# Performance work log

Measured on AMD Instinct MI355X. Metric: run time of the kernel, lower is better.

## Reference

```python
import jax, jax.numpy as jnp
import numpy as np

B, Q, C, V = 512, 100, 81, 117  # batch, queries, obj classes (80+no-object), verbs
THRES, ALPHA, BETA = 0.7, 1.0, 0.5


def setup_inputs() -> dict:
    key = jax.random.key(0)
    k1, k2, k3, k4, k5, k6 = jax.random.split(key, 6)
    out_obj_logits = jax.random.normal(k1, (B, Q, C), jnp.float32)
    out_verb_logits = jax.random.normal(k2, (B, Q, V), jnp.float32)
    out_sub_boxes = jax.random.uniform(k3, (B, Q, 4), jnp.float32)
    out_obj_boxes = jax.random.uniform(k4, (B, Q, 4), jnp.float32)
    # correct_mat: binary verb-object compatibility [V, C-1] + ones column for no-object slot -> [V, C]
    cm = (jax.random.uniform(k5, (V, C - 1)) < 0.3).astype(jnp.float32)
    correct_mat = jnp.concatenate([cm, jnp.ones((V, 1), jnp.float32)], axis=1)
    target_sizes = jax.random.randint(k6, (B, 2), 480, 1334).astype(jnp.int64)
    return {
        'out_obj_logits': out_obj_logits,
        'out_verb_logits': out_verb_logits,
        'out_sub_boxes': out_sub_boxes,
        'out_obj_boxes': out_obj_boxes,
        'correct_mat': correct_mat,
        'target_sizes': target_sizes,
    }


def _box_cxcywh_to_xyxy(b):
    cx, cy, w, h = b[..., 0], b[..., 1], b[..., 2], b[..., 3]
    return jnp.stack([cx - 0.5 * w, cy - 0.5 * h, cx + 0.5 * w, cy + 0.5 * h], axis=-1)


def _pairwise_iou(boxes):  # boxes [Q,4] xyxy (pixel coords, +1 convention as in source)
    x1, y1, x2, y2 = boxes[:, 0], boxes[:, 1], boxes[:, 2], boxes[:, 3]
    area = (x2 - x1 + 1.0) * (y2 - y1 + 1.0)
    xx1 = jnp.maximum(x1[:, None], x1[None, :])
    yy1 = jnp.maximum(y1[:, None], y1[None, :])
    xx2 = jnp.minimum(x2[:, None], x2[None, :])
    yy2 = jnp.minimum(y2[:, None], y2[None, :])
    w = jnp.maximum(0.0, xx2 - xx1 + 1.0)
    h = jnp.maximum(0.0, yy2 - yy1 + 1.0)
    inter = w * h
    union = area[:, None] + area[None, :] - inter
    return inter / union


def _nms_one_image(sub_b, obj_b, obj_lab, max_scores):
    # Greedy pairwise triplet NMS. Grouping key in the source degenerates to the
    # object label alone (subject cat is constant, verb-label string identical),
    # so suppression applies only between detections with the same object label.
    order = jnp.argsort(-max_scores)
    sb, ob, lab = sub_b[order], obj_b[order], obj_lab[order]
    ovr = jnp.power(_pairwise_iou(sb), ALPHA) * jnp.power(_pairwise_iou(ob), BETA)
    upper = jnp.triu(jnp.ones((Q, Q), bool), 1)
    sup_mat = upper & (lab[:, None] == lab[None, :]) & (ovr > THRES)

    def body(i, supp):
        return supp | (sup_mat[i] & jnp.logical_not(supp[i]))

    supp = jax.lax.fori_loop(0, Q, body, jnp.zeros((Q,), bool))
    keep = jnp.zeros((Q,), bool).at[order].set(jnp.logical_not(supp))
    return keep  # in original query order


def reference(out_obj_logits, out_verb_logits, out_sub_boxes, out_obj_boxes, correct_mat, target_sizes):
    obj_prob = jax.nn.softmax(out_obj_logits, axis=-1)
    obj_scores = obj_prob[..., :-1].max(axis=-1)            # [B,Q]
    obj_labels = obj_prob[..., :-1].argmax(axis=-1)         # [B,Q]
    verb_scores = jax.nn.sigmoid(out_verb_logits)           # [B,Q,V]

    ts = target_sizes.astype(jnp.float32)
    img_h, img_w = ts[:, 0], ts[:, 1]
    scale_fct = jnp.stack([img_w, img_h, img_w, img_h], axis=1)  # [B,4]
    sub_boxes = _box_cxcywh_to_xyxy(out_sub_boxes) * scale_fct[:, None, :]
    obj_boxes = _box_cxcywh_to_xyxy(out_obj_boxes) * scale_fct[:, None, :]

    # masks[b,q,v] = correct_mat[v, obj_labels[b,q]]
    masks = correct_mat.T[obj_labels]                        # [B,Q,V]
    hoi_scores = verb_scores * obj_scores[..., None] * masks

    max_scores = hoi_scores.max(axis=-1)                     # [B,Q]
    keep = jax.vmap(_nms_one_image)(sub_boxes, obj_boxes, obj_labels, max_scores)
    return hoi_scores, obj_labels, sub_boxes, obj_boxes, keep
```

## Files before the change

kernel.cpp:

```cpp
#include <hip/hip_runtime.h>
#include <math.h>

#define Bn 512
#define Qn 100
#define Cn 81
#define Vn 117
#define NQ (Bn * Qn)

#define OFF_HOI  0
#define OFF_LAB  (NQ * Vn)
#define OFF_SUB  (OFF_LAB + NQ)
#define OFF_OBJ  (OFF_SUB + NQ * 4)
#define OFF_KEEP (OFF_OBJ + NQ * 4)

__device__ __forceinline__ float frcp(float x) { return __builtin_amdgcn_rcpf(x); }

__global__ __launch_bounds__(512) void hoi_fused(
    const float* __restrict__ obj_logits,
    const float* __restrict__ verb_logits,
    const float* __restrict__ sub_boxes,
    const float* __restrict__ obj_boxes,
    const float* __restrict__ cm,
    const int*   __restrict__ target_sizes,
    float* __restrict__ out)
{
    __shared__ __align__(16) char smem[37920];
    __shared__ float sc[Qn];
    __shared__ int   labs[Qn];

    float*      CM    = (float*)smem;
    float4*     Ssub  = (float4*)smem;
    float4*     Sobj  = Ssub + Qn;
    float4*     Smeta = Sobj + Qn;
    ulonglong2* RR    = (ulonglong2*)(Smeta + Qn);

    const int tid = threadIdx.x;
    const int b   = blockIdx.x;

    {
        const float4* c4 = (const float4*)cm;
        float4* C4 = (float4*)CM;
        for (int i = tid; i < (Vn * Cn) / 4; i += 512) C4[i] = c4[i];
        if (tid == 0) CM[Vn * Cn - 1] = cm[Vn * Cn - 1];
    }

    float4 rs = make_float4(0.f, 0.f, 0.f, 0.f), ro = rs;
    if (tid < Qn) {
        const float ih = (float)target_sizes[2 * b + 0];
        const float iw = (float)target_sizes[2 * b + 1];
        const int idx = b * Qn + tid;
        float4 bx = ((const float4*)sub_boxes)[idx];
        rs.x = (bx.x - 0.5f * bx.z) * iw;
        rs.y = (bx.y - 0.5f * bx.w) * ih;
        rs.z = (bx.x + 0.5f * bx.z) * iw;
        rs.w = (bx.y + 0.5f * bx.w) * ih;
        ((float4*)(out + OFF_SUB))[idx] = rs;
        bx = ((const float4*)obj_boxes)[idx];
        ro.x = (bx.x - 0.5f * bx.z) * iw;
        ro.y = (bx.y - 0.5f * bx.w) * ih;
        ro.z = (bx.x + 0.5f * bx.z) * iw;
        ro.w = (bx.y + 0.5f * bx.w) * ih;
        ((float4*)(out + OFF_OBJ))[idx] = ro;
    }
    __syncthreads();

    {
        const int t = tid & 15;
        const int g = tid >> 4;
        for (int q = g; q < Qn; q += 32) {
            const size_t idx = (size_t)b * Qn + q;
            const float* lg = obj_logits + idx * Cn;
            const float* vl = verb_logits + idx * Vn;

            float l0 = lg[t], l1 = lg[t + 16], l2 = lg[t + 32],
                  l3 = lg[t + 48], l4 = lg[t + 64], l5 = lg[80];
            float w0 = vl[t], w1 = vl[t + 16], w2 = vl[t + 32], w3 = vl[t + 48],
                  w4 = vl[t + 64], w5 = vl[t + 80], w6 = vl[t + 96];
            float w7 = (t < 5) ? vl[112 + t] : 0.f;

            float v = l0; int vid = t;
            if (l1 > v) { v = l1; vid = t + 16; }
            if (l2 > v) { v = l2; vid = t + 32; }
            if (l3 > v) { v = l3; vid = t + 48; }
            if (l4 > v) { v = l4; vid = t + 64; }
            #pragma unroll
            for (int o = 8; o; o >>= 1) {
                float ov = __shfl_xor(v, o, 64);
                int   oi = __shfl_xor(vid, o, 64);
                if (ov > v || (ov == v && oi < vid)) { v = ov; vid = oi; }
            }

            float e = __expf(l0) + __expf(l1) + __expf(l2) + __expf(l3) + __expf(l4);
            #pragma unroll
            for (int o = 8; o; o >>= 1) e += __shfl_xor(e, o, 64);
            e += __expf(l5);

            const int   label     = vid;
            const float obj_score = __expf(v) * frcp(e);

            float* hout = out + OFF_HOI + idx * Vn;
            const float* cmrow = CM + label;
            float mx = 0.f;
            {
                float h;
                h = frcp(1.f + __expf(-w0)) * obj_score * cmrow[(t      ) * Cn];
                hout[t      ] = h; mx = fmaxf(mx, h);
                h = frcp(1.f + __expf(-w1)) * obj_score * cmrow[(t +  16) * Cn];
                hout[t +  16] = h; mx = fmaxf(mx, h);
                h = frcp(1.f + __expf(-w2)) * obj_score * cmrow[(t +  32) * Cn];
                hout[t +  32] = h; mx = fmaxf(mx, h);
                h = frcp(1.f + __expf(-w3)) * obj_score * cmrow[(t +  48) * Cn];
                hout[t +  48] = h; mx = fmaxf(mx, h);
                h = frcp(1.f + __expf(-w4)) * obj_score * cmrow[(t +  64) * Cn];
                hout[t +  64] = h; mx = fmaxf(mx, h);
                h = frcp(1.f + __expf(-w5)) * obj_score * cmrow[(t +  80) * Cn];
                hout[t +  80] = h; mx = fmaxf(mx, h);
                h = frcp(1.f + __expf(-w6)) * obj_score * cmrow[(t +  96) * Cn];
                hout[t +  96] = h; mx = fmaxf(mx, h);
                if (t < 5) {
                    h = frcp(1.f + __expf(-w7)) * obj_score * cmrow[(112 + t) * Cn];
                    hout[112 + t] = h; mx = fmaxf(mx, h);
                }
            }
            #pragma unroll
            for (int o = 8; o; o >>= 1) mx = fmaxf(mx, __shfl_xor(mx, o, 64));

            if (t == 0) {
                out[OFF_LAB + idx] = (float)label;
                sc[q]   = mx;
                labs[q] = label;
            }
        }
    }
    __syncthreads();

    if (tid < Qn) {
        const float kv = sc[tid];
        int r = 0;
        #pragma unroll 4
        for (int j = 0; j < Qn; j++) {
            float sj = sc[j];
            r += (sj > kv) || (sj == kv && j < tid);
        }
        Ssub[r] = rs;
        Sobj[r] = ro;
        Smeta[r] = make_float4((rs.z - rs.x + 1.f) * (rs.w - rs.y + 1.f),
                               (ro.z - ro.x + 1.f) * (ro.w - ro.y + 1.f),
                               (float)labs[tid], (float)tid);
    }
    __syncthreads();

    {
        const int tc   = tid & 127;
        const int uq   = tid >> 7;
        const int lane = tid & 63;
        const int sub  = (tid >> 6) & 1;
        const bool jv  = (tc < Qn);

        float4 js = make_float4(0.f, 0.f, 0.f, 0.f), jo = js, jm = js;
        if (jv) { js = Ssub[tc]; jo = Sobj[tc]; jm = Smeta[tc]; }

        const int i0 = 25 * uq;
        const int i1 = (25 * uq + 25 < Qn - 1) ? 25 * uq + 25 : Qn - 1;
        for (int i = i0; i < i1; i++) {
            float4 is = Ssub[i], io = Sobj[i], im = Smeta[i];
            float ww = fmaxf(0.f, fminf(is.z, js.z) - fmaxf(is.x, js.x) + 1.f);
            float hh = fmaxf(0.f, fminf(is.w, js.w) - fmaxf(is.y, js.y) + 1.f);
            float inter = ww * hh;
            float iou_s = inter / (im.x + jm.x - inter);
            ww = fmaxf(0.f, fminf(io.z, jo.z) - fmaxf(io.x, jo.x) + 1.f);
            hh = fmaxf(0.f, fminf(io.w, jo.w) - fmaxf(io.y, jo.y) + 1.f);
            inter = ww * hh;
            float iou_o = inter / (im.y + jm.y - inter);
            bool cond = jv && (tc > i) && (jm.z == im.z) && (iou_s * sqrtf(iou_o) > 0.7f);
            unsigned long long m = __ballot(cond);
            if (lane == 0) ((unsigned long long*)&RR[i])[sub] = m;
        }
    }
    __syncthreads();

    if (tid < 64) {
        unsigned long long s0 = 0ull, s1 = 0ull;
        ulonglong2 r = RR[0];
        for (int k = 0; k < Qn - 1; k++) {
            ulonglong2 rn = RR[(k + 1 < Qn - 1) ? k + 1 : k];
            unsigned long long dead = ((k < 64 ? s0 : s1) >> (k & 63)) & 1ull;
            if (!dead) { s0 |= r.x; s1 |= r.y; }
            r = rn;
        }
        float* keepp = out + OFF_KEEP + (size_t)b * Qn;
        keepp[(int)Smeta[tid].w] = ((s0 >> tid) & 1ull) ? 0.f : 1.f;
        if (tid < 36)
            keepp[(int)Smeta[64 + tid].w] = ((s1 >> tid) & 1ull) ? 0.f : 1.f;
    }
}

extern "C" void kernel_launch(void* const* d_in, const int* in_sizes, int n_in,
                              void* d_out, int out_size, void* d_ws, size_t ws_size,
                              hipStream_t stream) {
    const float* obj_logits   = (const float*)d_in[0];
    const float* verb_logits  = (const float*)d_in[1];
    const float* sub_boxes    = (const float*)d_in[2];
    const float* obj_boxes    = (const float*)d_in[3];
    const float* correct_mat  = (const float*)d_in[4];
    const int*   target_sizes = (const int*)d_in[5];
    float* out = (float*)d_out;
    (void)d_ws; (void)ws_size; (void)in_sizes; (void)n_in; (void)out_size;

    hoi_fused<<<Bn, 512, 0, stream>>>(obj_logits, verb_logits, sub_boxes,
                                      obj_boxes, correct_mat, target_sizes, out);
}
```

Baseline: 120.4 us.

## Split fused kernel into per-query scoring kernel and per-image NMS kernel

Replaces the single per-image kernel with two launches: a scoring kernel that spreads the 51200 queries over many small blocks (16 queries per 256-thread block) and reads correct_mat directly from global memory, and a separate NMS kernel that reloads boxes, labels and max scores from the output buffer. The aim is to remove the large per-block shared-memory copy of correct_mat and the serial query loop, which limited occupancy and parallelism. The max scores are staged temporarily in the keep slot, which the NMS kernel then overwrites. The cost is an extra launch and a global round-trip for the intermediates. The NMS pairwise loop also software-prefetches the next row and uses 256 threads.

```diff
diff --git a/kernel.cpp b/kernel.cpp
--- a/kernel.cpp
+++ b/kernel.cpp
@@ -15,7 +15,7 @@
 
 __device__ __forceinline__ float frcp(float x) { return __builtin_amdgcn_rcpf(x); }
 
-__global__ __launch_bounds__(512) void hoi_fused(
+__global__ __launch_bounds__(256) void hoi_score(
     const float* __restrict__ obj_logits,
     const float* __restrict__ verb_logits,
     const float* __restrict__ sub_boxes,
@@ -24,129 +24,109 @@
     const int*   __restrict__ target_sizes,
     float* __restrict__ out)
 {
-    __shared__ __align__(16) char smem[37920];
-    __shared__ float sc[Qn];
-    __shared__ int   labs[Qn];
+    const int tid = threadIdx.x;
+    const int t   = tid & 15;
+    const int g   = tid >> 4;
+    const int idx = blockIdx.x * 16 + g;
+    const int b   = idx / Qn;
 
-    float*      CM    = (float*)smem;
-    float4*     Ssub  = (float4*)smem;
-    float4*     Sobj  = Ssub + Qn;
-    float4*     Smeta = Sobj + Qn;
-    ulonglong2* RR    = (ulonglong2*)(Smeta + Qn);
-
-    const int tid = threadIdx.x;
-    const int b   = blockIdx.x;
-
-    {
-        const float4* c4 = (const float4*)cm;
-        float4* C4 = (float4*)CM;
-        for (int i = tid; i < (Vn * Cn) / 4; i += 512) C4[i] = c4[i];
-        if (tid == 0) CM[Vn * Cn - 1] = cm[Vn * Cn - 1];
+    if (t < 2) {
+        const float ih = (float)target_sizes[2 * b + 0];
+        const float iw = (float)target_sizes[2 * b + 1];
+        const float4 bx = ((const float4*)(t == 0 ? sub_boxes : obj_boxes))[idx];
+        float4 r;
+        r.x = (bx.x - 0.5f * bx.z) * iw;
+        r.y = (bx.y - 0.5f * bx.w) * ih;
+        r.z = (bx.x + 0.5f * bx.z) * iw;
+        r.w = (bx.y + 0.5f * bx.w) * ih;
+        ((float4*)(out + (t == 0 ? OFF_SUB : OFF_OBJ)))[idx] = r;
     }
 
-    float4 rs = make_float4(0.f, 0.f, 0.f, 0.f), ro = rs;
+    const float* lg = obj_logits + (size_t)idx * Cn;
+    const float* vl = verb_logits + (size_t)idx * Vn;
+
+    float l0 = lg[t], l1 = lg[t + 16], l2 = lg[t + 32],
+          l3 = lg[t + 48], l4 = lg[t + 64], l5 = lg[80];
+    float w0 = vl[t], w1 = vl[t + 16], w2 = vl[t + 32], w3 = vl[t + 48],
+          w4 = vl[t + 64], w5 = vl[t + 80], w6 = vl[t + 96];
+    float w7 = (t < 5) ? vl[112 + t] : 0.f;
+
+    float v = l0; int vid = t;
+    if (l1 > v) { v = l1; vid = t + 16; }
+    if (l2 > v) { v = l2; vid = t + 32; }
+    if (l3 > v) { v = l3; vid = t + 48; }
+    if (l4 > v) { v = l4; vid = t + 64; }
+    #pragma unroll
+    for (int o = 8; o; o >>= 1) {
+        float ov = __shfl_xor(v, o, 64);
+        int   oi = __shfl_xor(vid, o, 64);
+        if (ov > v || (ov == v && oi < vid)) { v = ov; vid = oi; }
+    }
+
+    float e = __expf(l0) + __expf(l1) + __expf(l2) + __expf(l3) + __expf(l4);
+    #pragma unroll
+    for (int o = 8; o; o >>= 1) e += __shfl_xor(e, o, 64);
+    e += __expf(l5);
+
+    const int   label     = vid;
+    const float obj_score = __expf(v) * frcp(e);
+
+    float* hout = out + OFF_HOI + (size_t)idx * Vn;
+    const float* cmrow = cm + label;
+    float mx = 0.f, h;
+    h = frcp(1.f + __expf(-w0)) * obj_score * cmrow[(t      ) * Cn]; hout[t      ] = h; mx = fmaxf(mx, h);
+    h = frcp(1.f + __expf(-w1)) * obj_score * cmrow[(t +  16) * Cn]; hout[t +  16] = h; mx = fmaxf(mx, h);
+    h = frcp(1.f + __expf(-w2)) * obj_score * cmrow[(t +  32) * Cn]; hout[t +  32] = h; mx = fmaxf(mx, h);
+    h = frcp(1.f + __expf(-w3)) * obj_score * cmrow[(t +  48) * Cn]; hout[t +  48] = h; mx = fmaxf(mx, h);
+    h = frcp(1.f + __expf(-w4)) * obj_score * cmrow[(t +  64) * Cn]; hout[t +  64] = h; mx = fmaxf(mx, h);
+    h = frcp(1.f + __expf(-w5)) * obj_score * cmrow[(t +  80) * Cn]; hout[t +  80] = h; mx = fmaxf(mx, h);
+    h = frcp(1.f + __expf(-w6)) * obj_score * cmrow[(t +  96) * Cn]; hout[t +  96] = h; mx = fmaxf(mx, h);
+    if (t < 5) {
+        h = frcp(1.f + __expf(-w7)) * obj_score * cmrow[(112 + t) * Cn];
+        hout[112 + t] = h; mx = fmaxf(mx, h);
+    }
+    #pragma unroll
+    for (int o = 8; o; o >>= 1) mx = fmaxf(mx, __shfl_xor(mx, o, 64));
+
+    if (t == 0) {
+        out[OFF_LAB + idx]  = (float)label;
+        out[OFF_KEEP + idx] = mx;
+    }
+}
+
+__global__ __launch_bounds__(256) void hoi_nms(float* __restrict__ out)
+{
+    __shared__ float  sc[Qn];
+    __shared__ float4 Ssub[Qn], Sobj[Qn], Smeta[Qn];
+    __shared__ ulonglong2 RR[Qn];
+
+    const int b   = blockIdx.x;
+    const int tid = threadIdx.x;
+
+    float  kv = 0.f, labf = 0.f;
+    float4 sb = make_float4(0.f, 0.f, 0.f, 0.f), ob = sb;
     if (tid < Qn) {
-        const float ih = (float)target_sizes[2 * b + 0];
-        const float iw = (float)target_sizes[2 * b + 1];
         const int idx = b * Qn + tid;
-        float4 bx = ((const float4*)sub_boxes)[idx];
-        rs.x = (bx.x - 0.5f * bx.z) * iw;
-        rs.y = (bx.y - 0.5f * bx.w) * ih;
-        rs.z = (bx.x + 0.5f * bx.z) * iw;
-        rs.w = (bx.y + 0.5f * bx.w) * ih;
-        ((float4*)(out + OFF_SUB))[idx] = rs;
-        bx = ((const float4*)obj_boxes)[idx];
-        ro.x = (bx.x - 0.5f * bx.z) * iw;
-        ro.y = (bx.y - 0.5f * bx.w) * ih;
-        ro.z = (bx.x + 0.5f * bx.z) * iw;
-        ro.w = (bx.y + 0.5f * bx.w) * ih;
-        ((float4*)(out + OFF_OBJ))[idx] = ro;
-    }
-    __syncthreads();
-
-    {
-        const int t = tid & 15;
-        const int g = tid >> 4;
-        for (int q = g; q < Qn; q += 32) {
-            const size_t idx = (size_t)b * Qn + q;
-            const float* lg = obj_logits + idx * Cn;
-            const float* vl = verb_logits + idx * Vn;
-
-            float l0 = lg[t], l1 = lg[t + 16], l2 = lg[t + 32],
-                  l3 = lg[t + 48], l4 = lg[t + 64], l5 = lg[80];
-            float w0 = vl[t], w1 = vl[t + 16], w2 = vl[t + 32], w3 = vl[t + 48],
-                  w4 = vl[t + 64], w5 = vl[t + 80], w6 = vl[t + 96];
-            float w7 = (t < 5) ? vl[112 + t] : 0.f;
-
-            float v = l0; int vid = t;
-            if (l1 > v) { v = l1; vid = t + 16; }
-            if (l2 > v) { v = l2; vid = t + 32; }
-            if (l3 > v) { v = l3; vid = t + 48; }
-            if (l4 > v) { v = l4; vid = t + 64; }
-            #pragma unroll
-            for (int o = 8; o; o >>= 1) {
-                float ov = __shfl_xor(v, o, 64);
-                int   oi = __shfl_xor(vid, o, 64);
-                if (ov > v || (ov == v && oi < vid)) { v = ov; vid = oi; }
-            }
-
-            float e = __expf(l0) + __expf(l1) + __expf(l2) + __expf(l3) + __expf(l4);
-            #pragma unroll
-            for (int o = 8; o; o >>= 1) e += __shfl_xor(e, o, 64);
-            e += __expf(l5);
-
-            const int   label     = vid;
-            const float obj_score = __expf(v) * frcp(e);
-
-            float* hout = out + OFF_HOI + idx * Vn;
-            const float* cmrow = CM + label;
-            float mx = 0.f;
-            {
-                float h;
-                h = frcp(1.f + __expf(-w0)) * obj_score * cmrow[(t      ) * Cn];
-                hout[t      ] = h; mx = fmaxf(mx, h);
-                h = frcp(1.f + __expf(-w1)) * obj_score * cmrow[(t +  16) * Cn];
-                hout[t +  16] = h; mx = fmaxf(mx, h);
-                h = frcp(1.f + __expf(-w2)) * obj_score * cmrow[(t +  32) * Cn];
-                hout[t +  32] = h; mx = fmaxf(mx, h);
-                h = frcp(1.f + __expf(-w3)) * obj_score * cmrow[(t +  48) * Cn];
-                hout[t +  48] = h; mx = fmaxf(mx, h);
-                h = frcp(1.f + __expf(-w4)) * obj_score * cmrow[(t +  64) * Cn];
-                hout[t +  64] = h; mx = fmaxf(mx, h);
-                h = frcp(1.f + __expf(-w5)) * obj_score * cmrow[(t +  80) * Cn];
-                hout[t +  80] = h; mx = fmaxf(mx, h);
-                h = frcp(1.f + __expf(-w6)) * obj_score * cmrow[(t +  96) * Cn];
-                hout[t +  96] = h; mx = fmaxf(mx, h);
-                if (t < 5) {
-                    h = frcp(1.f + __expf(-w7)) * obj_score * cmrow[(112 + t) * Cn];
-                    hout[112 + t] = h; mx = fmaxf(mx, h);
-                }
-            }
-            #pragma unroll
-            for (int o = 8; o; o >>= 1) mx = fmaxf(mx, __shfl_xor(mx, o, 64));
-
-            if (t == 0) {
-                out[OFF_LAB + idx] = (float)label;
-                sc[q]   = mx;
-                labs[q] = label;
-            }
-        }
+        kv   = out[OFF_KEEP + idx];
+        sb   = ((const float4*)(out + OFF_SUB))[idx];
+        ob   = ((const float4*)(out + OFF_OBJ))[idx];
+        labf = out[OFF_LAB + idx];
+        sc[tid] = kv;
     }
     __syncthreads();
 
     if (tid < Qn) {
-        const float kv = sc[tid];
         int r = 0;
         #pragma unroll 4
         for (int j = 0; j < Qn; j++) {
             float sj = sc[j];
             r += (sj > kv) || (sj == kv && j < tid);
         }
-        Ssub[r] = rs;
-        Sobj[r] = ro;
-        Smeta[r] = make_float4((rs.z - rs.x + 1.f) * (rs.w - rs.y + 1.f),
-                               (ro.z - ro.x + 1.f) * (ro.w - ro.y + 1.f),
-                               (float)labs[tid], (float)tid);
+        Ssub[r] = sb;
+        Sobj[r] = ob;
+        Smeta[r] = make_float4((sb.z - sb.x + 1.f) * (sb.w - sb.y + 1.f),
+                               (ob.z - ob.x + 1.f) * (ob.w - ob.y + 1.f),
+                               labf, (float)tid);
     }
     __syncthreads();
 
@@ -160,10 +140,12 @@
         float4 js = make_float4(0.f, 0.f, 0.f, 0.f), jo = js, jm = js;
         if (jv) { js = Ssub[tc]; jo = Sobj[tc]; jm = Smeta[tc]; }
 
-        const int i0 = 25 * uq;
-        const int i1 = (25 * uq + 25 < Qn - 1) ? 25 * uq + 25 : Qn - 1;
+        const int i0 = uq * 50;
+        const int i1 = (i0 + 50 < Qn - 1) ? i0 + 50 : Qn - 1;
+        float4 is = Ssub[i0], io = Sobj[i0], im = Smeta[i0];
         for (int i = i0; i < i1; i++) {
-            float4 is = Ssub[i], io = Sobj[i], im = Smeta[i];
+            const int inx = (i + 1 < i1) ? i + 1 : i;
+            float4 isn = Ssub[inx], ion = Sobj[inx], imn = Smeta[inx];
             float ww = fmaxf(0.f, fminf(is.z, js.z) - fmaxf(is.x, js.x) + 1.f);
             float hh = fmaxf(0.f, fminf(is.w, js.w) - fmaxf(is.y, js.y) + 1.f);
             float inter = ww * hh;
@@ -175,6 +157,7 @@
             bool cond = jv && (tc > i) && (jm.z == im.z) && (iou_s * sqrtf(iou_o) > 0.7f);
             unsigned long long m = __ballot(cond);
             if (lane == 0) ((unsigned long long*)&RR[i])[sub] = m;
+            is = isn; io = ion; im = imn;
         }
     }
     __syncthreads();
@@ -207,6 +190,7 @@
     float* out = (float*)d_out;
     (void)d_ws; (void)ws_size; (void)in_sizes; (void)n_in; (void)out_size;
 
-    hoi_fused<<<Bn, 512, 0, stream>>>(obj_logits, verb_logits, sub_boxes,
-                                      obj_boxes, correct_mat, target_sizes, out);
+    hoi_score<<<NQ / 16, 256, 0, stream>>>(obj_logits, verb_logits, sub_boxes,
+                                           obj_boxes, correct_mat, target_sizes, out);
+    hoi_nms<<<Bn, 256, 0, stream>>>(out);
 }
```

Measured after the change: 130.3 us. 1.08x slower.

## Transpose compatibility matrix in LDS and process one query per wavefront with vector loads

Applied to the files above, without the earlier changes.

The correct_mat is now stored transposed in shared memory with a padded row stride, so each label's verb row is contiguous and can be read as float4. The per-query work moves from 16-thread groups to a full 64-lane wavefront, with each lane doing unaligned 4-wide loads and stores of logits and HOI scores. The aim is fewer memory instructions and no strided LDS gathers. In exchange most lanes sit idle (only 20 or 30 of 64 are active), the reductions take more shuffle steps, and the transpose fill uses scalar stores with an integer divide.

```diff
diff --git a/kernel.cpp b/kernel.cpp
--- a/kernel.cpp
+++ b/kernel.cpp
@@ -6,6 +6,7 @@
 #define Cn 81
 #define Vn 117
 #define NQ (Bn * Qn)
+#define CMP 120
 
 #define OFF_HOI  0
 #define OFF_LAB  (NQ * Vn)
@@ -14,6 +15,13 @@
 #define OFF_KEEP (OFF_OBJ + NQ * 4)
 
 __device__ __forceinline__ float frcp(float x) { return __builtin_amdgcn_rcpf(x); }
+
+__device__ __forceinline__ float4 ld4u(const float* p) {
+    float4 r; __builtin_memcpy(&r, p, 16); return r;
+}
+__device__ __forceinline__ void st4u(float* p, const float4& v) {
+    __builtin_memcpy(p, &v, 16);
+}
 
 __global__ __launch_bounds__(512) void hoi_fused(
     const float* __restrict__ obj_logits,
@@ -24,11 +32,11 @@
     const int*   __restrict__ target_sizes,
     float* __restrict__ out)
 {
-    __shared__ __align__(16) char smem[37920];
+    __shared__ __align__(16) char smem[Cn * CMP * 4];
     __shared__ float sc[Qn];
     __shared__ int   labs[Qn];
 
-    float*      CM    = (float*)smem;
+    float*      CMT   = (float*)smem;
     float4*     Ssub  = (float4*)smem;
     float4*     Sobj  = Ssub + Qn;
     float4*     Smeta = Sobj + Qn;
@@ -37,11 +45,9 @@
     const int tid = threadIdx.x;
     const int b   = blockIdx.x;
 
-    {
-        const float4* c4 = (const float4*)cm;
-        float4* C4 = (float4*)CM;
-        for (int i = tid; i < (Vn * Cn) / 4; i += 512) C4[i] = c4[i];
-        if (tid == 0) CM[Vn * Cn - 1] = cm[Vn * Cn - 1];
+    for (int i = tid; i < Vn * Cn; i += 512) {
+        const int v = i / Cn, c = i - v * Cn;
+        CMT[c * CMP + v] = cm[i];
     }
 
     float4 rs = make_float4(0.f, 0.f, 0.f, 0.f), ro = rs;
@@ -65,67 +71,68 @@
     __syncthreads();
 
     {
-        const int t = tid & 15;
-        const int g = tid >> 4;
-        for (int q = g; q < Qn; q += 32) {
-            const size_t idx = (size_t)b * Qn + q;
+        const int w = tid >> 6;
+        const int l = tid & 63;
+        const size_t bQ = (size_t)b * Qn;
+
+        for (int q = w; q < Qn; q += 8) {
+            const size_t idx = bQ + q;
             const float* lg = obj_logits + idx * Cn;
             const float* vl = verb_logits + idx * Vn;
 
-            float l0 = lg[t], l1 = lg[t + 16], l2 = lg[t + 32],
-                  l3 = lg[t + 48], l4 = lg[t + 64], l5 = lg[80];
-            float w0 = vl[t], w1 = vl[t + 16], w2 = vl[t + 32], w3 = vl[t + 48],
-                  w4 = vl[t + 64], w5 = vl[t + 80], w6 = vl[t + 96];
-            float w7 = (t < 5) ? vl[112 + t] : 0.f;
-
-            float v = l0; int vid = t;
-            if (l1 > v) { v = l1; vid = t + 16; }
-            if (l2 > v) { v = l2; vid = t + 32; }
-            if (l3 > v) { v = l3; vid = t + 48; }
-            if (l4 > v) { v = l4; vid = t + 64; }
+            float a0 = -1e30f, a1 = -1e30f, a2 = -1e30f, a3 = -1e30f;
+            if (l < 20) {
+                float4 r = ld4u(lg + 4 * l);
+                a0 = r.x; a1 = r.y; a2 = r.z; a3 = r.w;
+            }
+            const float l80 = lg[80];
+
+            float4 wv = make_float4(0.f, 0.f, 0.f, 0.f);
+            float  w116 = 0.f;
+            if (l < 29) wv = ld4u(vl + 4 * l);
+            else if (l == 29) w116 = vl[116];
+
+            float v = a0; int vid = 4 * l;
+            if (a1 > v) { v = a1; vid = 4 * l + 1; }
+            if (a2 > v) { v = a2; vid = 4 * l + 2; }
+            if (a3 > v) { v = a3; vid = 4 * l + 3; }
             #pragma unroll
-            for (int o = 8; o; o >>= 1) {
+            for (int o = 32; o; o >>= 1) {
                 float ov = __shfl_xor(v, o, 64);
                 int   oi = __shfl_xor(vid, o, 64);
                 if (ov > v || (ov == v && oi < vid)) { v = ov; vid = oi; }
             }
 
-            float e = __expf(l0) + __expf(l1) + __expf(l2) + __expf(l3) + __expf(l4);
+            float e = 0.f;
+            if (l < 20) e = __expf(a0) + __expf(a1) + __expf(a2) + __expf(a3);
             #pragma unroll
-            for (int o = 8; o; o >>= 1) e += __shfl_xor(e, o, 64);
-            e += __expf(l5);
+            for (int o = 32; o; o >>= 1) e += __shfl_xor(e, o, 64);
+            e += __expf(l80);
 
             const int   label     = vid;
             const float obj_score = __expf(v) * frcp(e);
 
             float* hout = out + OFF_HOI + idx * Vn;
-            const float* cmrow = CM + label;
+            const float* crow = CMT + label * CMP;
             float mx = 0.f;
-            {
-                float h;
-                h = frcp(1.f + __expf(-w0)) * obj_score * cmrow[(t      ) * Cn];
-                hout[t      ] = h; mx = fmaxf(mx, h);
-                h = frcp(1.f + __expf(-w1)) * obj_score * cmrow[(t +  16) * Cn];
-                hout[t +  16] = h; mx = fmaxf(mx, h);
-                h = frcp(1.f + __expf(-w2)) * obj_score * cmrow[(t +  32) * Cn];
-                hout[t +  32] = h; mx = fmaxf(mx, h);
-                h = frcp(1.f + __expf(-w3)) * obj_score * cmrow[(t +  48) * Cn];
-                hout[t +  48] = h; mx = fmaxf(mx, h);
-                h = frcp(1.f + __expf(-w4)) * obj_score * cmrow[(t +  64) * Cn];
-                hout[t +  64] = h; mx = fmaxf(mx, h);
-                h = frcp(1.f + __expf(-w5)) * obj_score * cmrow[(t +  80) * Cn];
-                hout[t +  80] = h; mx = fmaxf(mx, h);
-                h = frcp(1.f + __expf(-w6)) * obj_score * cmrow[(t +  96) * Cn];
-                hout[t +  96] = h; mx = fmaxf(mx, h);
-                if (t < 5) {
-                    h = frcp(1.f + __expf(-w7)) * obj_score * cmrow[(112 + t) * Cn];
-                    hout[112 + t] = h; mx = fmaxf(mx, h);
-                }
+            if (l < 29) {
+                float4 cv = *(const float4*)(crow + 4 * l);
+                float4 h;
+                h.x = frcp(1.f + __expf(-wv.x)) * obj_score * cv.x;
+                h.y = frcp(1.f + __expf(-wv.y)) * obj_score * cv.y;
+                h.z = frcp(1.f + __expf(-wv.z)) * obj_score * cv.z;
+                h.w = frcp(1.f + __expf(-wv.w)) * obj_score * cv.w;
+                st4u(hout + 4 * l, h);
+                mx = fmaxf(fmaxf(h.x, h.y), fmaxf(h.z, h.w));
+            } else if (l == 29) {
+                float h = frcp(1.f + __expf(-w116)) * obj_score * crow[116];
+                hout[116] = h;
+                mx = h;
             }
             #pragma unroll
-            for (int o = 8; o; o >>= 1) mx = fmaxf(mx, __shfl_xor(mx, o, 64));
-
-            if (t == 0) {
+            for (int o = 32; o; o >>= 1) mx = fmaxf(mx, __shfl_xor(mx, o, 64));
+
+            if (l == 0) {
                 out[OFF_LAB + idx] = (float)label;
                 sc[q]   = mx;
                 labs[q] = label;
```

After: 135.1 us. 1.12x slower.

## Stage logits through LDS with coalesced float4 loads and bitmask correct_mat

Applied to the files above, without the earlier changes.

Copies each image's object and verb logits into shared memory with coalesced float4 loads, and stores the HOI scores back to global memory the same way. Replaces the per-block float copy of correct_mat with a per-label 117-bit mask built by shared-memory atomicOr. Per-query softmax and sigmoid work now runs one thread per query (100 threads) instead of 16-lane groups, which cuts parallelism in the compute phases and adds LDS bank conflicts from strided row access. The writeback is overlapped with the NMS ranking step.

```diff
diff --git a/kernel.cpp b/kernel.cpp
--- a/kernel.cpp
+++ b/kernel.cpp
@@ -24,25 +24,16 @@
     const int*   __restrict__ target_sizes,
     float* __restrict__ out)
 {
-    __shared__ __align__(16) char smem[37920];
-    __shared__ float sc[Qn];
-    __shared__ int   labs[Qn];
-
-    float*      CM    = (float*)smem;
-    float4*     Ssub  = (float4*)smem;
-    float4*     Sobj  = Ssub + Qn;
-    float4*     Smeta = Sobj + Qn;
-    ulonglong2* RR    = (ulonglong2*)(Smeta + Qn);
+    __shared__ __align__(16) float R1[Qn * Vn];
+    __shared__ unsigned long long CMB[Cn][2];
+    __shared__ float  sc[Qn];
+    __shared__ float4 Ssub[Qn], Sobj[Qn], Smeta[Qn];
+    __shared__ ulonglong2 RR[Qn];
 
     const int tid = threadIdx.x;
     const int b   = blockIdx.x;
 
-    {
-        const float4* c4 = (const float4*)cm;
-        float4* C4 = (float4*)CM;
-        for (int i = tid; i < (Vn * Cn) / 4; i += 512) C4[i] = c4[i];
-        if (tid == 0) CM[Vn * Cn - 1] = cm[Vn * Cn - 1];
-    }
+    if (tid < Cn) { CMB[tid][0] = 0ull; CMB[tid][1] = 0ull; }
 
     float4 rs = make_float4(0.f, 0.f, 0.f, 0.f), ro = rs;
     if (tid < Qn) {
@@ -65,72 +56,60 @@
     __syncthreads();
 
     {
-        const int t = tid & 15;
-        const int g = tid >> 4;
-        for (int q = g; q < Qn; q += 32) {
-            const size_t idx = (size_t)b * Qn + q;
-            const float* lg = obj_logits + idx * Cn;
-            const float* vl = verb_logits + idx * Vn;
+        const float4* cm4 = (const float4*)cm;
+        for (int i = tid; i < (Vn * Cn) / 4; i += 512) {
+            float4 f = cm4[i];
+            const int e0 = 4 * i;
+            if (f.x != 0.f) { int v = (e0    ) / Cn, c = (e0    ) - v * Cn; atomicOr(&CMB[c][v >> 6], 1ull << (v & 63)); }
+            if (f.y != 0.f) { int v = (e0 + 1) / Cn, c = (e0 + 1) - v * Cn; atomicOr(&CMB[c][v >> 6], 1ull << (v & 63)); }
+            if (f.z != 0.f) { int v = (e0 + 2) / Cn, c = (e0 + 2) - v * Cn; atomicOr(&CMB[c][v >> 6], 1ull << (v & 63)); }
+            if (f.w != 0.f) { int v = (e0 + 3) / Cn, c = (e0 + 3) - v * Cn; atomicOr(&CMB[c][v >> 6], 1ull << (v & 63)); }
+        }
+        if (tid == 0 && cm[Vn * Cn - 1] != 0.f)
+            atomicOr(&CMB[Cn - 1][116 >> 6], 1ull << (116 & 63));
 
-            float l0 = lg[t], l1 = lg[t + 16], l2 = lg[t + 32],
-                  l3 = lg[t + 48], l4 = lg[t + 64], l5 = lg[80];
-            float w0 = vl[t], w1 = vl[t + 16], w2 = vl[t + 32], w3 = vl[t + 48],
-                  w4 = vl[t + 64], w5 = vl[t + 80], w6 = vl[t + 96];
-            float w7 = (t < 5) ? vl[112 + t] : 0.f;
+        const float4* o4 = (const float4*)(obj_logits + (size_t)b * Qn * Cn);
+        float4* r4 = (float4*)R1;
+        for (int i = tid; i < (Qn * Cn) / 4; i += 512) r4[i] = o4[i];
+    }
+    __syncthreads();
 
-            float v = l0; int vid = t;
-            if (l1 > v) { v = l1; vid = t + 16; }
-            if (l2 > v) { v = l2; vid = t + 32; }
-            if (l3 > v) { v = l3; vid = t + 48; }
-            if (l4 > v) { v = l4; vid = t + 64; }
-            #pragma unroll
-            for (int o = 8; o; o >>= 1) {
-                float ov = __shfl_xor(v, o, 64);
-                int   oi = __shfl_xor(vid, o, 64);
-                if (ov > v || (ov == v && oi < vid)) { v = ov; vid = oi; }
-            }
+    int   label  = 0;
+    float oscore = 0.f;
+    if (tid < Qn) {
+        const float* L = R1 + tid * Cn;
+        float vmax = -1e30f; int vid = 0; float e = 0.f;
+        for (int c = 0; c < 80; ++c) {
+            float x = L[c];
+            e += __expf(x);
+            if (x > vmax) { vmax = x; vid = c; }
+        }
+        e += __expf(L[80]);
+        label  = vid;
+        oscore = __expf(vmax) * frcp(e);
+    }
+    __syncthreads();
 
-            float e = __expf(l0) + __expf(l1) + __expf(l2) + __expf(l3) + __expf(l4);
-            #pragma unroll
-            for (int o = 8; o; o >>= 1) e += __shfl_xor(e, o, 64);
-            e += __expf(l5);
+    {
+        const float4* v4 = (const float4*)(verb_logits + (size_t)b * Qn * Vn);
+        float4* r4 = (float4*)R1;
+        for (int i = tid; i < (Qn * Vn) / 4; i += 512) r4[i] = v4[i];
+    }
+    __syncthreads();
 
-            const int   label     = vid;
-            const float obj_score = __expf(v) * frcp(e);
-
-            float* hout = out + OFF_HOI + idx * Vn;
-            const float* cmrow = CM + label;
-            float mx = 0.f;
-            {
-                float h;
-                h = frcp(1.f + __expf(-w0)) * obj_score * cmrow[(t      ) * Cn];
-                hout[t      ] = h; mx = fmaxf(mx, h);
-                h = frcp(1.f + __expf(-w1)) * obj_score * cmrow[(t +  16) * Cn];
-                hout[t +  16] = h; mx = fmaxf(mx, h);
-                h = frcp(1.f + __expf(-w2)) * obj_score * cmrow[(t +  32) * Cn];
-                hout[t +  32] = h; mx = fmaxf(mx, h);
-                h = frcp(1.f + __expf(-w3)) * obj_score * cmrow[(t +  48) * Cn];
-                hout[t +  48] = h; mx = fmaxf(mx, h);
-                h = frcp(1.f + __expf(-w4)) * obj_score * cmrow[(t +  64) * Cn];
-                hout[t +  64] = h; mx = fmaxf(mx, h);
-                h = frcp(1.f + __expf(-w5)) * obj_score * cmrow[(t +  80) * Cn];
-                hout[t +  80] = h; mx = fmaxf(mx, h);
-                h = frcp(1.f + __expf(-w6)) * obj_score * cmrow[(t +  96) * Cn];
-                hout[t +  96] = h; mx = fmaxf(mx, h);
-                if (t < 5) {
-                    h = frcp(1.f + __expf(-w7)) * obj_score * cmrow[(112 + t) * Cn];
-                    hout[112 + t] = h; mx = fmaxf(mx, h);
-                }
-            }
-            #pragma unroll
-            for (int o = 8; o; o >>= 1) mx = fmaxf(mx, __shfl_xor(mx, o, 64));
-
-            if (t == 0) {
-                out[OFF_LAB + idx] = (float)label;
-                sc[q]   = mx;
-                labs[q] = label;
-            }
+    if (tid < Qn) {
+        float* Wr = R1 + tid * Vn;
+        const unsigned long long m0 = CMB[label][0], m1 = CMB[label][1];
+        float mx = 0.f;
+        for (int v = 0; v < Vn; ++v) {
+            float x = Wr[v];
+            bool on = ((v < 64 ? (m0 >> v) : (m1 >> (v - 64))) & 1ull);
+            float h = on ? frcp(1.f + __expf(-x)) * oscore : 0.f;
+            Wr[v] = h;
+            mx = fmaxf(mx, h);
         }
+        sc[tid] = mx;
+        out[OFF_LAB + b * Qn + tid] = (float)label;
     }
     __syncthreads();
 
@@ -146,7 +125,11 @@
         Sobj[r] = ro;
         Smeta[r] = make_float4((rs.z - rs.x + 1.f) * (rs.w - rs.y + 1.f),
                                (ro.z - ro.x + 1.f) * (ro.w - ro.y + 1.f),
-                               (float)labs[tid], (float)tid);
+                               (float)label, (float)tid);
+    } else {
+        float4* ho = (float4*)(out + OFF_HOI + (size_t)b * Qn * Vn);
+        const float4* r4 = (const float4*)R1;
+        for (int i = tid - Qn; i < (Qn * Vn) / 4; i += 512 - Qn) ho[i] = r4[i];
     }
     __syncthreads();
 
```

Measured after the change: 125.8 us. +4.4%, slower.
